# Performance work log

Measured on AMD Instinct MI355X. Metric: run time of the kernel, lower is better.

Reference implementation:

```python
import jax, jax.numpy as jnp
import numpy as np
import math

B, N, D = 2, 4096, 1024
NUM_LAYERS = 12
INIT_RANGE = 0.02


def setup_inputs() -> dict:
    key = jax.random.key(0)
    k1, k2 = jax.random.split(key)
    hidden_states = jax.random.normal(k1, (B, N, D), dtype=jnp.float32)
    std = INIT_RANGE / math.sqrt(2.0 * NUM_LAYERS * D)
    queries = jax.random.normal(k2, (D, D), dtype=jnp.float32) * std
    return {"hidden_states": hidden_states, "queries": queries}


def reference(hidden_states, queries):
    # Q = F.linear(X, W) = X @ W^T  -> [B, N, D]
    q = jnp.einsum('bnd,ed->bne', hidden_states, queries)
    # pre_attn = Q @ X^T  -> [B, N, N]
    pre_attn = jnp.einsum('bne,bme->bnm', q, hidden_states)
    # attention = pre_attn @ X  -> [B, N, D]
    attention = jnp.einsum('bnm,bmd->bnd', pre_attn, hidden_states)
    return attention
```

## Files before the change

kernel.cpp:

```cpp
#include <hip/hip_runtime.h>
#include <hip/hip_bf16.h>
#include <stdint.h>

using bf16 = __hip_bfloat16;
typedef __attribute__((ext_vector_type(8))) short short8;
typedef __attribute__((ext_vector_type(4))) float f32x4;

#define BM 128
#define BK 32

__device__ __forceinline__ void g2lds16(const void* g, void* l) {
    __builtin_amdgcn_global_load_lds(
        (const __attribute__((address_space(1))) void*)g,
        (__attribute__((address_space(3))) void*)l,
        16, 0, 0);
}

template <int N>
__device__ __forceinline__ void s_wait_vmcnt() {
    asm volatile("s_waitcnt vmcnt(%0)" :: "n"(N) : "memory");
}
__device__ __forceinline__ void s_wait_lgkm0() {
    asm volatile("s_waitcnt lgkmcnt(0)" ::: "memory");
    __builtin_amdgcn_sched_barrier(0);
}

__device__ __forceinline__ short f2bs(float x) {
    union { bf16 h; short s; } u;
    u.h = __float2bfloat16(x);
    return u.s;
}

__device__ __forceinline__ int bswz(int row, int cg) { return cg ^ ((row >> 1) & 3); }
__device__ __forceinline__ int fswz(int row, int cg) { return cg ^ (row & 7); }

__global__ __launch_bounds__(256)
void transpose_cvt(const float* __restrict__ src, ushort* __restrict__ dstT,
                   ushort* __restrict__ dstN,
                   int R, int C, long sstride, long dstrideT, long dstrideN)
{
    __shared__ __align__(16) ushort t[64][72];
    const float* s = src + (size_t)blockIdx.z * sstride;
    ushort*      dT = dstT + (size_t)blockIdx.z * dstrideT;
    const int r0 = blockIdx.y * 64, c0 = blockIdx.x * 64;
    const int tid = threadIdx.x;
#pragma unroll
    for (int ii = 0; ii < 4; ++ii) {
        int idx = ii * 256 + tid;
        int r = idx >> 4, c4 = (idx & 15) * 4;
        float4 v = *(const float4*)&s[(size_t)(r0 + r) * C + c0 + c4];
        union { ushort u[4]; uint2 q; } o;
        o.u[0] = (ushort)f2bs(v.x); o.u[1] = (ushort)f2bs(v.y);
        o.u[2] = (ushort)f2bs(v.z); o.u[3] = (ushort)f2bs(v.w);
        *(uint2*)&t[r][c4] = o.q;
        if (dstN) {
            ushort* dN = dstN + (size_t)blockIdx.z * dstrideN;
            *(uint2*)&dN[(size_t)(r0 + r) * C + c0 + c4] = o.q;
        }
    }
    __syncthreads();
#pragma unroll
    for (int ii = 0; ii < 2; ++ii) {
        int idx = ii * 256 + tid;
        int c = idx >> 3, r8 = (idx & 7) * 8;
        union { ushort u[8]; uint4 v; } tmp;
#pragma unroll
        for (int j = 0; j < 8; ++j) tmp.u[j] = t[r8 + j][c];
        *(uint4*)&dT[(size_t)(c0 + c) * R + r0 + r8] = tmp.v;
    }
}

template <int MODE, int A_F32, int NFRAG>
__global__ __launch_bounds__(256)
void gemm_bt(const void* __restrict__ Av, const bf16* __restrict__ B,
             void* __restrict__ Cv, int M, int N, int K, int kChunks,
             long sA, long sB, long sC)
{
    constexpr int BN  = 32 * NFRAG;
    constexpr int BSH = BN / 64;
    constexpr int ASH = A_F32 ? 4 : 2;
    constexpr int L   = ASH + BSH;
    constexpr int ANE = BM * BK * (A_F32 ? 2 : 1);
    __shared__ __align__(16) bf16 lA[3][ANE];
    __shared__ __align__(16) bf16 lB[3][BN * BK];

    const int z     = blockIdx.z;
    const int batch = z / kChunks;
    const int chunk = z - batch * kChunks;
    const int kLen  = K / kChunks;
    const int k0    = chunk * kLen;

    const int gx  = gridDim.x;
    int flat = blockIdx.y * gx + blockIdx.x;
    const int cpx = (gx * gridDim.y) >> 3;
    flat = (flat & 7) * cpx + (flat >> 3);
    const int m0 = (flat / gx) * BM;
    const int n0 = (flat - (flat / gx) * gx) * BN;

    const int tid  = threadIdx.x;
    const int lane = tid & 63;
    const int wave = tid >> 6;
    const int wr   = wave >> 1, wc = wave & 1;
    const int ml   = lane & 15;
    const int q    = lane >> 4;

    const bf16* Bb = B + (size_t)batch * sB;
    const bf16* bp[BSH];
#pragma unroll
    for (int s = 0; s < BSH; ++s) {
        int idx = s * 256 + tid;
        int row = idx >> 2, cg = idx & 3;
        bp[s] = Bb + (size_t)(n0 + row) * K + k0 + 8 * bswz(row, cg);
    }

    const float* a32[4];
    const bf16*  a16[2];
    if constexpr (A_F32) {
        const float* Ab = (const float*)Av + (size_t)batch * sA;
#pragma unroll
        for (int s = 0; s < 4; ++s) {
            int idx = s * 256 + tid;
            int row = idx >> 3, cg = idx & 7;
            a32[s] = Ab + (size_t)(m0 + row) * K + k0 + 4 * fswz(row, cg);
        }
    } else {
        const bf16* Ab = (const bf16*)Av + (size_t)batch * sA;
#pragma unroll
        for (int s = 0; s < 2; ++s) {
            int idx = s * 256 + tid;
            int row = idx >> 2, cg = idx & 3;
            a16[s] = Ab + (size_t)(m0 + row) * K + k0 + 8 * bswz(row, cg);
        }
    }

    f32x4 acc[4][NFRAG] = {};

    auto stage = [&](int buf) {
        if constexpr (A_F32) {
            float* lAf = (float*)lA[buf];
#pragma unroll
            for (int s = 0; s < 4; ++s) {
                g2lds16(a32[s], &lAf[(s * 256 + tid) * 4]);
                a32[s] += BK;
            }
        } else {
#pragma unroll
            for (int s = 0; s < 2; ++s) {
                g2lds16(a16[s], &lA[buf][(s * 256 + tid) * 8]);
                a16[s] += BK;
            }
        }
#pragma unroll
        for (int s = 0; s < BSH; ++s) {
            g2lds16(bp[s], &lB[buf][(s * 256 + tid) * 8]);
            bp[s] += BK;
        }
    };

    auto step = [&](int buf, bool doStage) {
        const bf16* cA = lA[buf];
        const bf16* cB = lB[buf];
        short8 af[4], bfr[NFRAG];
#pragma unroll
        for (int i = 0; i < 4; ++i) {
            const int rA = wr * 64 + i * 16 + ml;
            if constexpr (A_F32) {
                const float* lAf = (const float*)cA;
                float4 x0 = *(const float4*)&lAf[rA * 32 + 4 * fswz(rA, 2 * q)];
                float4 x1 = *(const float4*)&lAf[rA * 32 + 4 * fswz(rA, 2 * q + 1)];
                af[i][0] = f2bs(x0.x); af[i][1] = f2bs(x0.y);
                af[i][2] = f2bs(x0.z); af[i][3] = f2bs(x0.w);
                af[i][4] = f2bs(x1.x); af[i][5] = f2bs(x1.y);
                af[i][6] = f2bs(x1.z); af[i][7] = f2bs(x1.w);
            } else {
                af[i] = *(const short8*)&cA[rA * 32 + 8 * bswz(rA, q)];
            }
        }
#pragma unroll
        for (int j = 0; j < NFRAG; ++j) {
            const int rB = wc * (16 * NFRAG) + j * 16 + ml;
            bfr[j] = *(const short8*)&cB[rB * 32 + 8 * bswz(rB, q)];
        }
        s_wait_lgkm0();
        __builtin_amdgcn_s_barrier();
        if (doStage) stage(buf);
        __builtin_amdgcn_s_setprio(1);
#pragma unroll
        for (int mi = 0; mi < 4; ++mi)
#pragma unroll
            for (int nj = 0; nj < NFRAG; ++nj)
                acc[mi][nj] = __builtin_amdgcn_mfma_f32_16x16x32_bf16(
                    af[mi], bfr[nj], acc[mi][nj], 0, 0, 0);
        __builtin_amdgcn_s_setprio(0);
    };

    const int nk = kLen / BK;
    stage(0); stage(1); stage(2);
    int cur = 0;
    for (int kt = 0; kt < nk - 2; ++kt) {
        s_wait_vmcnt<2 * L>();
        __builtin_amdgcn_s_barrier();
        step(cur, kt < nk - 3);
        cur = (cur == 2) ? 0 : cur + 1;
    }
    s_wait_vmcnt<L>();
    __builtin_amdgcn_s_barrier();
    step(cur, false);
    cur = (cur == 2) ? 0 : cur + 1;
    s_wait_vmcnt<0>();
    __builtin_amdgcn_s_barrier();
    step(cur, false);

#pragma unroll
    for (int mi = 0; mi < 4; ++mi)
#pragma unroll
        for (int nj = 0; nj < NFRAG; ++nj)
#pragma unroll
            for (int r = 0; r < 4; ++r) {
                int row = m0 + wr * 64 + mi * 16 + q * 4 + r;
                int col = n0 + wc * (16 * NFRAG) + nj * 16 + ml;
                if constexpr (MODE == 1) {
                    float* Cf = (float*)Cv + (size_t)batch * sC;
                    atomicAdd(&Cf[(size_t)row * N + col], acc[mi][nj][r]);
                } else if constexpr (MODE == 0) {
                    ushort* Cb = (ushort*)Cv + (size_t)batch * sC;
                    Cb[(size_t)row * N + col] = (ushort)f2bs(acc[mi][nj][r]);
                } else {
                    float* Cf = (float*)Cv + (size_t)batch * sC;
                    Cf[(size_t)row * N + col] = acc[mi][nj][r];
                }
            }
}

extern "C" void kernel_launch(void* const* d_in, const int* in_sizes, int n_in,
                              void* d_out, int out_size, void* d_ws, size_t ws_size,
                              hipStream_t stream)
{
    const int B = 2, N = 4096, D = 1024;
    const float* X = (const float*)d_in[0];
    const float* W = (const float*)d_in[1];
    float* out = (float*)d_out;

    char* ob = (char*)d_out;
    char* ws = (char*)d_ws;
    ushort* Xt = (ushort*)ob;
    float*  Gf = (float*)(ob + (16ll << 20));
    ushort* Wt = (ushort*)(ob + (28ll << 20));

    const bool bigws = ws_size >= (20ull << 20);
    ushort* Xb = bigws ? (ushort*)ws : nullptr;
    ushort* Mt = (ushort*)(ws + (bigws ? (16ll << 20) : 0));

    transpose_cvt<<<dim3(D / 64, N / 64, B), 256, 0, stream>>>(
        X, Xt, Xb, N, D, (long)N * D, (long)D * N, (long)N * D);
    transpose_cvt<<<dim3(D / 64, D / 64, 1), 256, 0, stream>>>(
        W, Wt, nullptr, D, D, 0, 0, 0);
    (void)hipMemsetAsync(Gf, 0, (size_t)B * D * D * sizeof(float), stream);
    gemm_bt<1, 0, 4><<<dim3(D / 128, D / BM, B * 4), 256, 0, stream>>>(
        (const void*)Xt, (const bf16*)Xt, Gf, D, D, N, 4,
        (long)D * N, (long)D * N, (long)D * D);
    gemm_bt<0, 1, 2><<<dim3(D / 64, D / BM, B), 256, 0, stream>>>(
        (const void*)Gf, (const bf16*)Wt, Mt, D, D, D, 1,
        (long)D * D, 0, (long)D * D);
    if (bigws) {
        gemm_bt<2, 0, 4><<<dim3(D / 128, N / BM, B), 256, 0, stream>>>(
            (const void*)Xb, (const bf16*)Mt, out, N, D, D, 1,
            (long)N * D, (long)D * D, (long)N * D);
    } else {
        gemm_bt<2, 1, 4><<<dim3(D / 128, N / BM, B), 256, 0, stream>>>(
            (const void*)X, (const bf16*)Mt, out, N, D, D, 1,
            (long)N * D, (long)D * D, (long)N * D);
    }
}
```

Before: 182.6 us.

## Restructure GEMM pipeline to one barrier per step and retune split-K and tiles

Rewrites the GEMM main loop so each iteration waits on one stage, loads fragments, issues the next prefetch into the freed buffer and runs MFMAs, removing the second barrier and priority toggles. Increases split-K for the Gram GEMM, makes the second GEMM split-K with atomic float accumulation followed by a separate bf16 conversion kernel, and halves the N tile of the final GEMM. The goal is more parallelism for the small GEMMs and less synchronization per k-step, at the cost of extra memset, atomics, a conversion pass and lower reuse in the final GEMM.

```diff
diff --git a/kernel.cpp b/kernel.cpp
--- a/kernel.cpp
+++ b/kernel.cpp
@@ -19,10 +19,6 @@
 template <int N>
 __device__ __forceinline__ void s_wait_vmcnt() {
     asm volatile("s_waitcnt vmcnt(%0)" :: "n"(N) : "memory");
-}
-__device__ __forceinline__ void s_wait_lgkm0() {
-    asm volatile("s_waitcnt lgkmcnt(0)" ::: "memory");
-    __builtin_amdgcn_sched_barrier(0);
 }
 
 __device__ __forceinline__ short f2bs(float x) {
@@ -70,6 +66,18 @@
     }
 }
 
+__global__ __launch_bounds__(256)
+void cvt_f32_bf16(const float* __restrict__ in, ushort* __restrict__ out, int n4)
+{
+    int i = blockIdx.x * 256 + threadIdx.x;
+    if (i >= n4) return;
+    float4 v = ((const float4*)in)[i];
+    union { ushort u[4]; uint2 q; } o;
+    o.u[0] = (ushort)f2bs(v.x); o.u[1] = (ushort)f2bs(v.y);
+    o.u[2] = (ushort)f2bs(v.z); o.u[3] = (ushort)f2bs(v.w);
+    ((uint2*)out)[i] = o.q;
+}
+
 template <int MODE, int A_F32, int NFRAG>
 __global__ __launch_bounds__(256)
 void gemm_bt(const void* __restrict__ Av, const bf16* __restrict__ B,
@@ -81,8 +89,9 @@
     constexpr int ASH = A_F32 ? 4 : 2;
     constexpr int L   = ASH + BSH;
     constexpr int ANE = BM * BK * (A_F32 ? 2 : 1);
+    constexpr int BNE = BN * BK;
     __shared__ __align__(16) bf16 lA[3][ANE];
-    __shared__ __align__(16) bf16 lB[3][BN * BK];
+    __shared__ __align__(16) bf16 lB[3][BNE];
 
     const int z     = blockIdx.z;
     const int batch = z / kChunks;
@@ -157,10 +166,9 @@
         }
     };
 
-    auto step = [&](int buf, bool doStage) {
+    auto frags = [&](int buf, short8 (&af)[4], short8 (&bfr)[NFRAG]) {
         const bf16* cA = lA[buf];
         const bf16* cB = lB[buf];
-        short8 af[4], bfr[NFRAG];
 #pragma unroll
         for (int i = 0; i < 4; ++i) {
             const int rA = wr * 64 + i * 16 + ml;
@@ -181,35 +189,46 @@
             const int rB = wc * (16 * NFRAG) + j * 16 + ml;
             bfr[j] = *(const short8*)&cB[rB * 32 + 8 * bswz(rB, q)];
         }
-        s_wait_lgkm0();
-        __builtin_amdgcn_s_barrier();
-        if (doStage) stage(buf);
-        __builtin_amdgcn_s_setprio(1);
+    };
+
+    auto mfma = [&](short8 (&af)[4], short8 (&bfr)[NFRAG]) {
 #pragma unroll
         for (int mi = 0; mi < 4; ++mi)
 #pragma unroll
             for (int nj = 0; nj < NFRAG; ++nj)
                 acc[mi][nj] = __builtin_amdgcn_mfma_f32_16x16x32_bf16(
                     af[mi], bfr[nj], acc[mi][nj], 0, 0, 0);
-        __builtin_amdgcn_s_setprio(0);
     };
 
     const int nk = kLen / BK;
-    stage(0); stage(1); stage(2);
+    stage(0); stage(1);
     int cur = 0;
-    for (int kt = 0; kt < nk - 2; ++kt) {
-        s_wait_vmcnt<2 * L>();
+    for (int t = 0; t < nk - 2; ++t) {
+        s_wait_vmcnt<L>();
         __builtin_amdgcn_s_barrier();
-        step(cur, kt < nk - 3);
+        short8 af_[4], bf_[NFRAG];
+        frags(cur, af_, bf_);
+        int nb = cur + 2; nb = (nb >= 3) ? nb - 3 : nb;
+        stage(nb);
+        mfma(af_, bf_);
+        asm volatile("s_waitcnt lgkmcnt(0)" ::: "memory");
         cur = (cur == 2) ? 0 : cur + 1;
     }
-    s_wait_vmcnt<L>();
-    __builtin_amdgcn_s_barrier();
-    step(cur, false);
-    cur = (cur == 2) ? 0 : cur + 1;
-    s_wait_vmcnt<0>();
-    __builtin_amdgcn_s_barrier();
-    step(cur, false);
+    {
+        s_wait_vmcnt<L>();
+        __builtin_amdgcn_s_barrier();
+        short8 af_[4], bf_[NFRAG];
+        frags(cur, af_, bf_);
+        mfma(af_, bf_);
+        cur = (cur == 2) ? 0 : cur + 1;
+    }
+    {
+        s_wait_vmcnt<0>();
+        __builtin_amdgcn_s_barrier();
+        short8 af_[4], bf_[NFRAG];
+        frags(cur, af_, bf_);
+        mfma(af_, bf_);
+    }
 
 #pragma unroll
     for (int mi = 0; mi < 4; ++mi)
@@ -243,9 +262,10 @@
 
     char* ob = (char*)d_out;
     char* ws = (char*)d_ws;
-    ushort* Xt = (ushort*)ob;
-    float*  Gf = (float*)(ob + (16ll << 20));
-    ushort* Wt = (ushort*)(ob + (28ll << 20));
+    ushort* Xt  = (ushort*)ob;
+    float*  Mtf = (float*)ob;
+    float*  Gf  = (float*)(ob + (16ll << 20));
+    ushort* Wt  = (ushort*)(ob + (28ll << 20));
 
     const bool bigws = ws_size >= (20ull << 20);
     ushort* Xb = bigws ? (ushort*)ws : nullptr;
@@ -256,18 +276,21 @@
     transpose_cvt<<<dim3(D / 64, D / 64, 1), 256, 0, stream>>>(
         W, Wt, nullptr, D, D, 0, 0, 0);
     (void)hipMemsetAsync(Gf, 0, (size_t)B * D * D * sizeof(float), stream);
-    gemm_bt<1, 0, 4><<<dim3(D / 128, D / BM, B * 4), 256, 0, stream>>>(
-        (const void*)Xt, (const bf16*)Xt, Gf, D, D, N, 4,
+    gemm_bt<1, 0, 4><<<dim3(D / 128, D / BM, B * 8), 256, 0, stream>>>(
+        (const void*)Xt, (const bf16*)Xt, Gf, D, D, N, 8,
         (long)D * N, (long)D * N, (long)D * D);
-    gemm_bt<0, 1, 2><<<dim3(D / 64, D / BM, B), 256, 0, stream>>>(
-        (const void*)Gf, (const bf16*)Wt, Mt, D, D, D, 1,
+    (void)hipMemsetAsync(Mtf, 0, (size_t)B * D * D * sizeof(float), stream);
+    gemm_bt<1, 1, 2><<<dim3(D / 64, D / BM, B * 4), 256, 0, stream>>>(
+        (const void*)Gf, (const bf16*)Wt, Mtf, D, D, D, 4,
         (long)D * D, 0, (long)D * D);
+    cvt_f32_bf16<<<dim3((B * D * D / 4 + 255) / 256), 256, 0, stream>>>(
+        Mtf, Mt, B * D * D / 4);
     if (bigws) {
-        gemm_bt<2, 0, 4><<<dim3(D / 128, N / BM, B), 256, 0, stream>>>(
+        gemm_bt<2, 0, 2><<<dim3(D / 64, N / BM, B), 256, 0, stream>>>(
             (const void*)Xb, (const bf16*)Mt, out, N, D, D, 1,
             (long)N * D, (long)D * D, (long)N * D);
     } else {
-        gemm_bt<2, 1, 4><<<dim3(D / 128, N / BM, B), 256, 0, stream>>>(
+        gemm_bt<2, 1, 2><<<dim3(D / 64, N / BM, B), 256, 0, stream>>>(
             (const void*)X, (const bf16*)Mt, out, N, D, D, 1,
             (long)N * D, (long)D * D, (long)N * D);
     }
```

Result: slower. 227.5 us (+24.6%).
